# Kernel optimization log

Hardware: AMD Instinct MI355X
Metric: run time of the kernel (lower is better)

## Reference

```python
import jax, jax.numpy as jnp
import numpy as np

NUM_EXPERTS = 8
TOP_K = 2
N_EMBD = 1024
D_FFN = 2048  # 4*N_EMBD // TOP_K, already multiple of BLOCK_N=128
BLOCK_M = 128
NORM_TOPK = True


def setup_inputs() -> dict:
    key = jax.random.key(0)
    k1, k2, k3 = jax.random.split(key, 3)
    x = jax.random.normal(k1, (2, 2048, N_EMBD), dtype=jnp.float32)
    router_w = jax.random.normal(k2, (NUM_EXPERTS, N_EMBD), dtype=jnp.float32) * 0.02
    w1 = jax.random.normal(k3, (N_EMBD, D_FFN * NUM_EXPERTS), dtype=jnp.float32) * 0.02
    return {"x": x, "router_w": router_w, "w1": w1}


def reference(x, router_w, w1):
    B, S, H = x.shape
    x_flat = x.reshape(-1, H)                                   # [T, H]
    router_logits = x_flat @ router_w.T                         # [T, E]
    probs = jax.nn.softmax(router_logits.astype(jnp.float32), axis=-1)
    rweights, sel = jax.lax.top_k(probs, TOP_K)                 # [T, k]
    if NORM_TOPK:
        rweights = rweights / rweights.sum(axis=-1, keepdims=True)
    rweights = rweights.astype(x.dtype)

    # repeat_interleave tokens top_k times, then stable-sort by expert id
    x_rep = jnp.repeat(x_flat, TOP_K, axis=0)                   # [M, H]
    sel_rep = sel.reshape(-1)                                   # [M]
    rw_rep = rweights.reshape(-1, 1)                            # [M, 1]
    order = jnp.argsort(sel_rep, stable=True)                   # expert-sort permutation
    x_grouped = x_rep[order]                                    # [M, H]
    sel_sorted = sel_rep[order]                                 # [M]
    rw_sorted = rw_rep[order]                                   # [M, 1]

    M = x_grouped.shape[0]
    nblk = M // BLOCK_M                                         # M divisible by BLOCK_M by construction
    # SDD kernel: expert of the first row of each BLOCK_M block selects w1 slice
    block_expert = sel_sorted[::BLOCK_M]                        # [nblk] == col_indices_ptr
    w1e = w1.reshape(H, NUM_EXPERTS, D_FFN)                     # w1[:, e*D:(e+1)*D] == w1e[:, e, :]
    w_blk = jnp.take(w1e, block_expert, axis=1)                 # [H, nblk, D]
    x_blk = x_grouped.reshape(nblk, BLOCK_M, H)                 # [nblk, Bm, H]
    block_sparse = jnp.einsum('bmh,hbd->bmd', x_blk, w_blk).reshape(M, D_FFN)

    block_sparse = jax.nn.gelu(block_sparse, approximate=False) * rw_sorted
    return block_sparse, router_logits
```

## Files before the change

### kernel.cpp

```cpp
#include <hip/hip_runtime.h>
#include <hip/hip_bf16.h>
#include <cmath>

typedef float f32x16 __attribute__((ext_vector_type(16)));
typedef __bf16 bf16x8 __attribute__((ext_vector_type(8)));
typedef __bf16 bf16x4 __attribute__((ext_vector_type(4)));

#define NE 8
#define H 1024
#define DF 2048
#define WCOLS 16384
#define NTOK 4096
#define MROWS 8192
#define NBLK 64


typedef const __attribute__((address_space(1))) unsigned int glb_u32;
typedef __attribute__((address_space(3))) unsigned int lds_u32;

__device__ __forceinline__ void async_load16(const void* g, void* l) {
    __builtin_amdgcn_global_load_lds((glb_u32*)g, (lds_u32*)l, 16, 0, 0);
}

__global__ __launch_bounds__(256) void prep_kernel(
    const float* __restrict__ x, const float* __restrict__ rw,
    const float* __restrict__ w1,
    float* __restrict__ logits, int* __restrict__ sel, float* __restrict__ rwn,
    __bf16* __restrict__ xb, __bf16* __restrict__ Wt)
{
    __shared__ float tile[32][132];
    int b = blockIdx.x;
    int tid = threadIdx.x;
    if (b < 1024) {
        int tok  = b * 4 + (tid >> 6);
        int lane = tid & 63;
        const float* xr = x + (size_t)tok * H;
        __bf16* xbr = xb + (size_t)tok * H;
        float acc[NE];
#pragma unroll
        for (int e = 0; e < NE; ++e) acc[e] = 0.f;
#pragma unroll
        for (int it = 0; it < 4; ++it) {
            int k = (it * 64 + lane) * 4;
            float4 xv = *(const float4*)(xr + k);
            bf16x4 xc;
            xc[0] = (__bf16)xv.x; xc[1] = (__bf16)xv.y;
            xc[2] = (__bf16)xv.z; xc[3] = (__bf16)xv.w;
            *(bf16x4*)(xbr + k) = xc;
#pragma unroll
            for (int e = 0; e < NE; ++e) {
                float4 wv = *(const float4*)(rw + e * H + k);
                acc[e] += xv.x * wv.x + xv.y * wv.y + xv.z * wv.z + xv.w * wv.w;
            }
        }
#pragma unroll
        for (int e = 0; e < NE; ++e) {
            float v = acc[e];
#pragma unroll
            for (int off = 32; off > 0; off >>= 1) v += __shfl_xor(v, off, 64);
            acc[e] = v;
        }
        if (lane == 0) {
#pragma unroll
            for (int e = 0; e < NE; ++e) logits[tok * NE + e] = acc[e];
            int i1 = 0; float m1 = acc[0];
#pragma unroll
            for (int e = 1; e < NE; ++e) if (acc[e] > m1) { m1 = acc[e]; i1 = e; }
            int i2 = -1; float m2 = -INFINITY;
#pragma unroll
            for (int e = 0; e < NE; ++e) if (e != i1 && acc[e] > m2) { m2 = acc[e]; i2 = e; }
            float e2 = expf(m2 - m1);
            float inv = 1.f / (1.f + e2);
            sel[tok * 2]     = i1;  sel[tok * 2 + 1] = i2;
            rwn[tok * 2]     = inv; rwn[tok * 2 + 1] = e2 * inv;
        }
        return;
    }
    int g  = b - 1024;
    int c  = g >> 5;
    int kb = g & 31;
    int kk = tid >> 3;
    int cc = (tid & 7) * 16;
    const float* src = w1 + (size_t)(kb * 32 + kk) * WCOLS + c * 128 + cc;
#pragma unroll
    for (int i = 0; i < 4; ++i) {
        float4 v = *(const float4*)(src + i * 4);
        *(float4*)&tile[kk][cc + i * 4] = v;
    }
    __syncthreads();
    int n = tid >> 1, kc0 = (tid & 1) * 16;
    bf16x8 o0, o1;
#pragma unroll
    for (int i = 0; i < 8; ++i) {
        o0[i] = (__bf16)tile[kc0 + i][n];
        o1[i] = (__bf16)tile[kc0 + 8 + i][n];
    }
    size_t tile_id = (size_t)(c >> 1) * 32 + kb;
    int group  = (c & 1) * 4 + (n >> 5);
    int chunk0 = kc0 >> 3;
    __bf16* dst = Wt + tile_id * 8192 + group * 1024 + chunk0 * 256 + (n & 31) * 8;
    *(bf16x8*)dst         = o0;
    *(bf16x8*)(dst + 256) = o1;
}

__global__ __launch_bounds__(1024) void sort_kernel(
    const int* __restrict__ sel, const float* __restrict__ rwn,
    int* __restrict__ stok, float* __restrict__ srw, int* __restrict__ bexp)
{
    __shared__ int cnt[NE][1024];
    __shared__ int wtot[NE][2];
    __shared__ int ebase[NE + 1];
    int t = threadIdx.x;
    int selv[8];
    int lc[NE];
#pragma unroll
    for (int e = 0; e < NE; ++e) lc[e] = 0;
    int base = t * 8;
#pragma unroll
    for (int j = 0; j < 8; ++j) { selv[j] = sel[base + j]; lc[selv[j]]++; }
#pragma unroll
    for (int e = 0; e < NE; ++e) cnt[e][t] = lc[e];
    __syncthreads();
    int g = t >> 7, j = t & 127, jl = j & 63;
    int s = 0, pre[8];
#pragma unroll
    for (int i = 0; i < 8; ++i) { pre[i] = s; s += cnt[g][j * 8 + i]; }
    int inc = s;
#pragma unroll
    for (int d = 1; d < 64; d <<= 1) {
        int v = __shfl_up(inc, d, 64);
        if (jl >= d) inc += v;
    }
    if (jl == 63) wtot[g][j >> 6] = inc;
    __syncthreads();
    int add = (j >= 64) ? wtot[g][0] : 0;
    int excl = inc - s + add;
#pragma unroll
    for (int i = 0; i < 8; ++i) cnt[g][j * 8 + i] = excl + pre[i];
    __syncthreads();
    if (t == 0) {
        int acc = 0;
        for (int e = 0; e < NE; ++e) { ebase[e] = acc; acc += wtot[e][0] + wtot[e][1]; }
        ebase[NE] = acc;
    }
    __syncthreads();
    int off[NE];
#pragma unroll
    for (int e = 0; e < NE; ++e) off[e] = ebase[e] + cnt[e][t];
#pragma unroll
    for (int j2 = 0; j2 < 8; ++j2) {
        int i = base + j2;
        int e = selv[j2];
        int pos = off[e]++;
        stok[pos] = i >> 1;
        srw[pos]  = rwn[i];
    }
    __syncthreads();
    if (t < NBLK) {
        int r = t * 128;
        int e = 0;
        while (e < NE - 1 && r >= ebase[e + 1]) ++e;
        bexp[t] = e;
    }
}

__global__ __launch_bounds__(256, 2) void moe_gemm(
    const __bf16* __restrict__ xb, const __bf16* __restrict__ Wt,
    const int* __restrict__ stok, const float* __restrict__ srw,
    const int* __restrict__ bexp, float* __restrict__ out)
{
    __shared__ __align__(16) __bf16 As[2][4096];
    __shared__ __align__(16) __bf16 Bs[2][8192];
    __shared__ int   tokS[128];
    __shared__ float rwS[128];

    int g = blockIdx.x;
    int by  = (g & 7) * 8 + ((g >> 3) & 7);
    int bxp = g >> 6;
    int tid = threadIdx.x;
    if (tid < 128) {
        tokS[tid] = stok[by * 128 + tid];
        rwS[tid]  = srw[by * 128 + tid];
    }
    int e = bexp[by];
    __syncthreads();

    int lane = tid & 63;
    int wv   = tid >> 6;
    int l32  = lane & 31;
    int hi   = lane >> 5;

    const __bf16* aSrc = xb + (size_t)tokS[wv * 32 + l32] * H + hi * 8;
    __bf16* aDst0 = &As[0][wv * 1024 + lane * 8];
    __bf16* aDst1 = &As[1][wv * 1024 + lane * 8];

    const __bf16* bSrc = Wt + (size_t)(e * 8 + bxp) * 32 * 8192 + wv * 2048 + lane * 8;
    __bf16* bDst0 = &Bs[0][wv * 2048 + lane * 8];
    __bf16* bDst1 = &Bs[1][wv * 2048 + lane * 8];

    int wm = (wv & 1) * 64;
    int wn = (wv >> 1) * 128;
    int ag = (wv & 1) * 2;
    int bg = (wv >> 1) * 4;

    f32x16 acc[2][4];
#pragma unroll
    for (int i = 0; i < 2; ++i)
#pragma unroll
        for (int j = 0; j < 4; ++j)
#pragma unroll
            for (int r = 0; r < 16; ++r) acc[i][j][r] = 0.f;

#pragma unroll
    for (int j = 0; j < 2; ++j) async_load16(aSrc + j * 16, aDst0 + j * 512);
#pragma unroll
    for (int j = 0; j < 4; ++j) async_load16(bSrc + j * 512, bDst0 + j * 512);

    for (int kb = 0; kb < 32; ++kb) {
        int cur = kb & 1;
        __syncthreads();
        if (kb < 31) {
            const __bf16* aN = aSrc + (kb + 1) * 32;
            const __bf16* bN = bSrc + (size_t)(kb + 1) * 8192;
            __bf16* aD = cur ? aDst0 : aDst1;
            __bf16* bD = cur ? bDst0 : bDst1;
#pragma unroll
            for (int j = 0; j < 2; ++j) async_load16(aN + j * 16, aD + j * 512);
#pragma unroll
            for (int j = 0; j < 4; ++j) async_load16(bN + j * 512, bD + j * 512);
        }
        bf16x8 af[2][2], bfr[4][2];
#pragma unroll
        for (int h = 0; h < 2; ++h) {
#pragma unroll
            for (int ti = 0; ti < 2; ++ti)
                af[ti][h] = *(const bf16x8*)&As[cur][(ag + ti) * 1024 + (h * 2 + hi) * 256 + l32 * 8];
#pragma unroll
            for (int tj = 0; tj < 4; ++tj)
                bfr[tj][h] = *(const bf16x8*)&Bs[cur][(bg + tj) * 1024 + (h * 2 + hi) * 256 + l32 * 8];
        }
#pragma unroll
        for (int h = 0; h < 2; ++h)
#pragma unroll
            for (int ti = 0; ti < 2; ++ti)
#pragma unroll
                for (int tj = 0; tj < 4; ++tj)
                    acc[ti][tj] = __builtin_amdgcn_mfma_f32_32x32x16_bf16(
                        af[ti][h], bfr[tj][h], acc[ti][tj], 0, 0, 0);
    }

    int rowh = hi * 4;
#pragma unroll
    for (int ti = 0; ti < 2; ++ti)
#pragma unroll
        for (int reg = 0; reg < 16; ++reg) {
            int row = (reg & 3) + 8 * (reg >> 2) + rowh;
            int m = wm + ti * 32 + row;
            float rw = rwS[m];
            size_t ob = (size_t)(by * 128 + m) * DF + bxp * 256 + wn + l32;
#pragma unroll
            for (int tj = 0; tj < 4; ++tj) {
                float val = acc[ti][tj][reg];
                float u = 0.7978845608028654f * val * (1.f + 0.044715f * val * val);
                float t = __expf(-2.f * fabsf(u));
                float th = (1.f - t) / (1.f + t);
                th = u < 0.f ? -th : th;
                out[ob + tj * 32] = 0.5f * val * (1.f + th) * rw;
            }
        }
}

extern "C" void kernel_launch(void* const* d_in, const int* in_sizes, int n_in,
                              void* d_out, int out_size, void* d_ws, size_t ws_size,
                              hipStream_t stream) {
    (void)in_sizes; (void)n_in; (void)out_size; (void)ws_size;
    const float* x        = (const float*)d_in[0];
    const float* router_w = (const float*)d_in[1];
    const float* w1       = (const float*)d_in[2];
    float* out    = (float*)d_out;
    float* logits = out + (size_t)MROWS * DF;

    char* ws    = (char*)d_ws;
    int*   sel  = (int*)(ws);
    float* rwn  = (float*)(ws + 0x8000);
    int*   stok = (int*)(ws + 0x10000);
    float* srw  = (float*)(ws + 0x18000);
    int*   bexp = (int*)(ws + 0x20000);
    __bf16* xb  = (__bf16*)(ws + (1 << 20));
    __bf16* Wt  = (__bf16*)(ws + (1 << 20) + (8 << 20));

    prep_kernel<<<5120, 256, 0, stream>>>(x, router_w, w1, logits, sel, rwn, xb, Wt);
    sort_kernel<<<1, 1024, 0, stream>>>(sel, rwn, stok, srw, bexp);
    moe_gemm<<<512, 256, 0, stream>>>(xb, Wt, stok, srw, bexp, out);
}
```

Measured before the change: 188.1 us.

## Triple-buffer LDS tiles with explicit vmcnt waits and MFMA priority boost

Replaces the double-buffered A/B LDS tiles with a three-stage ring buffer. Global-to-LDS async loads are now issued two k-steps ahead, and each iteration waits with a partial s_waitcnt vmcnt(6) instead of a full drain. The MFMA block is wrapped in s_setprio to favour the math waves. The aim is to hide global load latency better, at the cost of more LDS per block (72 KB), which could limit occupancy.

Measured after the change: 191.2 us. No clear change (+1.7%).

```diff
diff --git a/kernel.cpp b/kernel.cpp
--- a/kernel.cpp
+++ b/kernel.cpp
@@ -169,8 +169,7 @@
     const int* __restrict__ stok, const float* __restrict__ srw,
     const int* __restrict__ bexp, float* __restrict__ out)
 {
-    __shared__ __align__(16) __bf16 As[2][4096];
-    __shared__ __align__(16) __bf16 Bs[2][8192];
+    __shared__ __align__(16) __bf16 smem[3 * 12288];
     __shared__ int   tokS[128];
     __shared__ float rwS[128];
 
@@ -191,12 +190,22 @@
     int hi   = lane >> 5;
 
     const __bf16* aSrc = xb + (size_t)tokS[wv * 32 + l32] * H + hi * 8;
-    __bf16* aDst0 = &As[0][wv * 1024 + lane * 8];
-    __bf16* aDst1 = &As[1][wv * 1024 + lane * 8];
-
     const __bf16* bSrc = Wt + (size_t)(e * 8 + bxp) * 32 * 8192 + wv * 2048 + lane * 8;
-    __bf16* bDst0 = &Bs[0][wv * 2048 + lane * 8];
-    __bf16* bDst1 = &Bs[1][wv * 2048 + lane * 8];
+    __bf16* aDst = smem + wv * 1024 + lane * 8;
+    __bf16* bDst = smem + 4096 + wv * 2048 + lane * 8;
+
+#define STAGE(kt, bb) do {                                                     \
+        const __bf16* aN = aSrc + (kt) * 32;                                   \
+        const __bf16* bN = bSrc + (size_t)(kt) * 8192;                         \
+        __bf16* aD = aDst + (bb) * 12288;                                      \
+        __bf16* bD = bDst + (bb) * 12288;                                      \
+        async_load16(aN,        aD);                                           \
+        async_load16(aN + 16,   aD + 512);                                     \
+        async_load16(bN,        bD);                                           \
+        async_load16(bN + 512,  bD + 512);                                     \
+        async_load16(bN + 1024, bD + 1024);                                    \
+        async_load16(bN + 1536, bD + 1536);                                    \
+    } while (0)
 
     int wm = (wv & 1) * 64;
     int wn = (wv >> 1) * 128;
@@ -211,34 +220,30 @@
 #pragma unroll
             for (int r = 0; r < 16; ++r) acc[i][j][r] = 0.f;
 
-#pragma unroll
-    for (int j = 0; j < 2; ++j) async_load16(aSrc + j * 16, aDst0 + j * 512);
-#pragma unroll
-    for (int j = 0; j < 4; ++j) async_load16(bSrc + j * 512, bDst0 + j * 512);
-
+    STAGE(0, 0);
+    STAGE(1, 1);
+
+    int cur = 0, nxt = 2;
     for (int kb = 0; kb < 32; ++kb) {
-        int cur = kb & 1;
-        __syncthreads();
-        if (kb < 31) {
-            const __bf16* aN = aSrc + (kb + 1) * 32;
-            const __bf16* bN = bSrc + (size_t)(kb + 1) * 8192;
-            __bf16* aD = cur ? aDst0 : aDst1;
-            __bf16* bD = cur ? bDst0 : bDst1;
-#pragma unroll
-            for (int j = 0; j < 2; ++j) async_load16(aN + j * 16, aD + j * 512);
-#pragma unroll
-            for (int j = 0; j < 4; ++j) async_load16(bN + j * 512, bD + j * 512);
-        }
+        if (kb < 31) asm volatile("s_waitcnt vmcnt(6)" ::: "memory");
+        else         asm volatile("s_waitcnt vmcnt(0)" ::: "memory");
+        __builtin_amdgcn_s_barrier();
+        __builtin_amdgcn_sched_barrier(0);
+        if (kb < 30) STAGE(kb + 2, nxt);
+
+        const __bf16* Ab = smem + cur * 12288;
+        const __bf16* Bb = Ab + 4096;
         bf16x8 af[2][2], bfr[4][2];
 #pragma unroll
         for (int h = 0; h < 2; ++h) {
 #pragma unroll
             for (int ti = 0; ti < 2; ++ti)
-                af[ti][h] = *(const bf16x8*)&As[cur][(ag + ti) * 1024 + (h * 2 + hi) * 256 + l32 * 8];
+                af[ti][h] = *(const bf16x8*)&Ab[(ag + ti) * 1024 + (h * 2 + hi) * 256 + l32 * 8];
 #pragma unroll
             for (int tj = 0; tj < 4; ++tj)
-                bfr[tj][h] = *(const bf16x8*)&Bs[cur][(bg + tj) * 1024 + (h * 2 + hi) * 256 + l32 * 8];
-        }
+                bfr[tj][h] = *(const bf16x8*)&Bb[(bg + tj) * 1024 + (h * 2 + hi) * 256 + l32 * 8];
+        }
+        __builtin_amdgcn_s_setprio(1);
 #pragma unroll
         for (int h = 0; h < 2; ++h)
 #pragma unroll
@@ -247,7 +252,12 @@
                 for (int tj = 0; tj < 4; ++tj)
                     acc[ti][tj] = __builtin_amdgcn_mfma_f32_32x32x16_bf16(
                         af[ti][h], bfr[tj][h], acc[ti][tj], 0, 0, 0);
-    }
+        __builtin_amdgcn_s_setprio(0);
+
+        cur = (cur == 2) ? 0 : cur + 1;
+        nxt = (nxt == 2) ? 0 : nxt + 1;
+    }
+#undef STAGE
 
     int rowh = hi * 4;
 #pragma unroll
```

## Restructure MoE GEMM to 8 waves with triple-buffered K=64 pipeline

Applied to the files above, without the earlier changes.

The GEMM kernel moves from 4 to 8 waves per block, so each wave now owns a 64x64 output sub-tile. K tiles grow to 64, and LDS is triple buffered so loads for stage kt+2 are issued while stage kt is computed. Synchronisation uses explicit vmcnt/lgkmcnt waits, raw barriers, sched_barrier and setprio around the MFMA bursts. This aims to hide global-load latency and raise MFMA utilisation, at the cost of more LDS (~144KB), more barriers per iteration, and lower per-wave arithmetic intensity.

New measurement: 191.1 us. About the same (+1.6%).

```diff
diff --git a/kernel.cpp b/kernel.cpp
--- a/kernel.cpp
+++ b/kernel.cpp
@@ -164,13 +164,12 @@
     }
 }
 
-__global__ __launch_bounds__(256, 2) void moe_gemm(
+__global__ __launch_bounds__(512, 2) void moe_gemm(
     const __bf16* __restrict__ xb, const __bf16* __restrict__ Wt,
     const int* __restrict__ stok, const float* __restrict__ srw,
     const int* __restrict__ bexp, float* __restrict__ out)
 {
-    __shared__ __align__(16) __bf16 As[2][4096];
-    __shared__ __align__(16) __bf16 Bs[2][8192];
+    __shared__ __align__(16) __bf16 smem[3 * 24576];
     __shared__ int   tokS[128];
     __shared__ float rwS[128];
 
@@ -189,65 +188,100 @@
     int wv   = tid >> 6;
     int l32  = lane & 31;
     int hi   = lane >> 5;
-
-    const __bf16* aSrc = xb + (size_t)tokS[wv * 32 + l32] * H + hi * 8;
-    __bf16* aDst0 = &As[0][wv * 1024 + lane * 8];
-    __bf16* aDst1 = &As[1][wv * 1024 + lane * 8];
-
-    const __bf16* bSrc = Wt + (size_t)(e * 8 + bxp) * 32 * 8192 + wv * 2048 + lane * 8;
-    __bf16* bDst0 = &Bs[0][wv * 2048 + lane * 8];
-    __bf16* bDst1 = &Bs[1][wv * 2048 + lane * 8];
-
-    int wm = (wv & 1) * 64;
-    int wn = (wv >> 1) * 128;
-    int ag = (wv & 1) * 2;
-    int bg = (wv >> 1) * 4;
-
-    f32x16 acc[2][4];
+    int wm2  = wv & 1;
+    int wn4  = wv >> 1;
+
+    int myTok = tokS[((tid >> 7) << 5) + (tid & 31)];
+    const __bf16* aSrcT = xb + (size_t)myTok * H + ((tid >> 5) & 3) * 8;
+    const __bf16* bSrcT = Wt + (size_t)(e * 8 + bxp) * 32 * 8192 + tid * 8;
+
+#define STAGE_HALF(kt_, bb_, h_) do {                                          \
+        __bf16* base_ = smem + (bb_) * 24576;                                  \
+        async_load16(aSrcT + (kt_) * 64 + (h_) * 32,                           \
+                     base_ + (h_) * 4096 + tid * 8);                           \
+        const __bf16* bs_ = bSrcT + (size_t)((kt_) * 2 + (h_)) * 8192;         \
+        __bf16* bd_ = base_ + 8192 + (h_) * 8192 + tid * 8;                    \
+        async_load16(bs_,        bd_);                                         \
+        async_load16(bs_ + 4096, bd_ + 4096);                                  \
+    } while (0)
+
+    int aRd = wm2 * 2048 + hi * 256 + l32 * 8;
+    int bRd = 8192 + wn4 * 2048 + hi * 256 + l32 * 8;
+
+    f32x16 acc[2][2];
 #pragma unroll
     for (int i = 0; i < 2; ++i)
 #pragma unroll
-        for (int j = 0; j < 4; ++j)
+        for (int j = 0; j < 2; ++j)
 #pragma unroll
             for (int r = 0; r < 16; ++r) acc[i][j][r] = 0.f;
 
-#pragma unroll
-    for (int j = 0; j < 2; ++j) async_load16(aSrc + j * 16, aDst0 + j * 512);
-#pragma unroll
-    for (int j = 0; j < 4; ++j) async_load16(bSrc + j * 512, bDst0 + j * 512);
-
-    for (int kb = 0; kb < 32; ++kb) {
-        int cur = kb & 1;
-        __syncthreads();
-        if (kb < 31) {
-            const __bf16* aN = aSrc + (kb + 1) * 32;
-            const __bf16* bN = bSrc + (size_t)(kb + 1) * 8192;
-            __bf16* aD = cur ? aDst0 : aDst1;
-            __bf16* bD = cur ? bDst0 : bDst1;
-#pragma unroll
-            for (int j = 0; j < 2; ++j) async_load16(aN + j * 16, aD + j * 512);
-#pragma unroll
-            for (int j = 0; j < 4; ++j) async_load16(bN + j * 512, bD + j * 512);
-        }
-        bf16x8 af[2][2], bfr[4][2];
-#pragma unroll
-        for (int h = 0; h < 2; ++h) {
+    STAGE_HALF(0, 0, 0); STAGE_HALF(0, 0, 1);
+    STAGE_HALF(1, 1, 0); STAGE_HALF(1, 1, 1);
+
+    int cur = 0;
+    for (int kt = 0; kt < 16; ++kt) {
+        if (kt < 15) asm volatile("s_waitcnt vmcnt(6)" ::: "memory");
+        else         asm volatile("s_waitcnt vmcnt(0)" ::: "memory");
+        __builtin_amdgcn_s_barrier();
+        __builtin_amdgcn_sched_barrier(0);
+        const __bf16* Ab = smem + cur * 24576;
+        int nb = cur + 2; if (nb >= 3) nb -= 3;
+
+        bf16x8 af[2][2], bfr[2][2];
+#pragma unroll
+        for (int s = 0; s < 2; ++s) {
+            int ao = aRd + s * 512;
+            int bo = bRd + s * 512;
+#pragma unroll
+            for (int ti = 0; ti < 2; ++ti) af[ti][s]  = *(const bf16x8*)&Ab[ao + ti * 1024];
+#pragma unroll
+            for (int tj = 0; tj < 2; ++tj) bfr[tj][s] = *(const bf16x8*)&Ab[bo + tj * 1024];
+        }
+        if (kt < 14) STAGE_HALF(kt + 2, nb, 0);
+        __builtin_amdgcn_s_barrier();
+        asm volatile("s_waitcnt lgkmcnt(0)" ::: "memory");
+        __builtin_amdgcn_sched_barrier(0);
+        __builtin_amdgcn_s_setprio(1);
+#pragma unroll
+        for (int s = 0; s < 2; ++s)
 #pragma unroll
             for (int ti = 0; ti < 2; ++ti)
-                af[ti][h] = *(const bf16x8*)&As[cur][(ag + ti) * 1024 + (h * 2 + hi) * 256 + l32 * 8];
-#pragma unroll
-            for (int tj = 0; tj < 4; ++tj)
-                bfr[tj][h] = *(const bf16x8*)&Bs[cur][(bg + tj) * 1024 + (h * 2 + hi) * 256 + l32 * 8];
-        }
-#pragma unroll
-        for (int h = 0; h < 2; ++h)
+#pragma unroll
+                for (int tj = 0; tj < 2; ++tj)
+                    acc[ti][tj] = __builtin_amdgcn_mfma_f32_32x32x16_bf16(
+                        af[ti][s], bfr[tj][s], acc[ti][tj], 0, 0, 0);
+        __builtin_amdgcn_s_setprio(0);
+        __builtin_amdgcn_s_barrier();
+
+#pragma unroll
+        for (int s = 0; s < 2; ++s) {
+            int ao = aRd + 4096 + s * 512;
+            int bo = bRd + 8192 + s * 512;
+#pragma unroll
+            for (int ti = 0; ti < 2; ++ti) af[ti][s]  = *(const bf16x8*)&Ab[ao + ti * 1024];
+#pragma unroll
+            for (int tj = 0; tj < 2; ++tj) bfr[tj][s] = *(const bf16x8*)&Ab[bo + tj * 1024];
+        }
+        if (kt < 14) STAGE_HALF(kt + 2, nb, 1);
+        __builtin_amdgcn_s_barrier();
+        asm volatile("s_waitcnt lgkmcnt(0)" ::: "memory");
+        __builtin_amdgcn_sched_barrier(0);
+        __builtin_amdgcn_s_setprio(1);
+#pragma unroll
+        for (int s = 0; s < 2; ++s)
 #pragma unroll
             for (int ti = 0; ti < 2; ++ti)
 #pragma unroll
-                for (int tj = 0; tj < 4; ++tj)
+                for (int tj = 0; tj < 2; ++tj)
                     acc[ti][tj] = __builtin_amdgcn_mfma_f32_32x32x16_bf16(
-                        af[ti][h], bfr[tj][h], acc[ti][tj], 0, 0, 0);
-    }
+                        af[ti][s], bfr[tj][s], acc[ti][tj], 0, 0, 0);
+        __builtin_amdgcn_s_setprio(0);
+        __builtin_amdgcn_s_barrier();
+
+        cur = cur + 1; if (cur >= 3) cur -= 3;
+    }
+#undef STAGE_HALF
 
     int rowh = hi * 4;
 #pragma unroll
@@ -255,11 +289,11 @@
 #pragma unroll
         for (int reg = 0; reg < 16; ++reg) {
             int row = (reg & 3) + 8 * (reg >> 2) + rowh;
-            int m = wm + ti * 32 + row;
+            int m = wm2 * 64 + ti * 32 + row;
             float rw = rwS[m];
-            size_t ob = (size_t)(by * 128 + m) * DF + bxp * 256 + wn + l32;
-#pragma unroll
-            for (int tj = 0; tj < 4; ++tj) {
+            size_t ob = (size_t)(by * 128 + m) * DF + bxp * 256 + wn4 * 64 + l32;
+#pragma unroll
+            for (int tj = 0; tj < 2; ++tj) {
                 float val = acc[ti][tj][reg];
                 float u = 0.7978845608028654f * val * (1.f + 0.044715f * val * val);
                 float t = __expf(-2.f * fabsf(u));
@@ -291,5 +325,5 @@
 
     prep_kernel<<<5120, 256, 0, stream>>>(x, router_w, w1, logits, sel, rwn, xb, Wt);
     sort_kernel<<<1, 1024, 0, stream>>>(sel, rwn, stok, srw, bexp);
-    moe_gemm<<<512, 256, 0, stream>>>(xb, Wt, stok, srw, bexp, out);
-}
+    moe_gemm<<<512, 512, 0, stream>>>(xb, Wt, stok, srw, bexp, out);
+}
```
